# Optimization experiments

Measured on AMD Instinct MI355X. Metric: run time of the kernel, lower is better.

The kernel has to match this reference:

```python
import jax, jax.numpy as jnp
import numpy as np

D_MODEL = 1024
N_HEADS = 16
D_HEAD = D_MODEL // N_HEADS
D_FF = 4 * D_MODEL
B, T = 2, 2048
LN_EPS = 1e-5


def layer_norm(x, g, b):
    mu = jnp.mean(x, axis=-1, keepdims=True)
    var = jnp.mean(jnp.square(x - mu), axis=-1, keepdims=True)
    return (x - mu) * jax.lax.rsqrt(var + LN_EPS) * g + b


def setup_inputs() -> dict:
    key = jax.random.key(0)
    ks = jax.random.split(key, 8)
    s = lambda fan: 1.0 / np.sqrt(fan)
    return {
        "x": jax.random.normal(ks[0], (B, T, D_MODEL), dtype=jnp.float32),
        "ln1_g": jnp.ones((D_MODEL,), jnp.float32),
        "ln1_b": jnp.zeros((D_MODEL,), jnp.float32),
        "Wqkv": jax.random.normal(ks[1], (D_MODEL, 3 * D_MODEL), jnp.float32) * s(D_MODEL),
        "Wout": jax.random.normal(ks[2], (D_MODEL, D_MODEL), jnp.float32) * s(D_MODEL),
        "ln2_g": jnp.ones((D_MODEL,), jnp.float32),
        "ln2_b": jnp.zeros((D_MODEL,), jnp.float32),
        "W1": jax.random.normal(ks[3], (D_MODEL, D_FF), jnp.float32) * s(D_MODEL),
        "b1": jnp.zeros((D_FF,), jnp.float32),
        "W2": jax.random.normal(ks[4], (D_FF, D_MODEL), jnp.float32) * s(D_FF),
        "b2": jnp.zeros((D_MODEL,), jnp.float32),
    }


def attention(x, Wqkv, Wout):
    Bx, Tx, C = x.shape
    qkv = x @ Wqkv  # [B,T,3C]
    q, k, v = jnp.split(qkv, 3, axis=-1)
    q = q.reshape(Bx, Tx, N_HEADS, D_HEAD)
    k = k.reshape(Bx, Tx, N_HEADS, D_HEAD)
    v = v.reshape(Bx, Tx, N_HEADS, D_HEAD)
    scores = jnp.einsum('bqhd,bkhd->bhqk', q, k) / np.sqrt(D_HEAD).astype(np.float32)
    causal = jnp.tril(jnp.ones((Tx, Tx), dtype=bool))
    scores = jnp.where(causal, scores, -jnp.inf)
    attn = jax.nn.softmax(scores, axis=-1)
    out = jnp.einsum('bhqk,bkhd->bqhd', attn, v).reshape(Bx, Tx, C)
    return out @ Wout


def reference(x, ln1_g, ln1_b, Wqkv, Wout, ln2_g, ln2_b, W1, b1, W2, b2):
    x = x + attention(layer_norm(x, ln1_g, ln1_b), Wqkv, Wout)
    h = layer_norm(x, ln2_g, ln2_b)
    h = jax.nn.gelu(h @ W1 + b1, approximate=False) @ W2 + b2
    return x + h
```

## Files before the change

kernel.cpp:

```cpp
#include <hip/hip_runtime.h>
#include <math.h>

typedef __bf16 bf16;
typedef __bf16 bf16x4 __attribute__((ext_vector_type(4)));
typedef __bf16 bf16x8 __attribute__((ext_vector_type(8)));
typedef float  f32x4  __attribute__((ext_vector_type(4)));

#define MFMA16(a,b,c) __builtin_amdgcn_mfma_f32_16x16x32_bf16((a),(b),(c),0,0,0)

static __device__ __forceinline__ bf16x8 combine8(const bf16* plo, const bf16* phi) {
  bf16x4 lo = *(const bf16x4*)plo;
  bf16x4 hi = *(const bf16x4*)phi;
  return __builtin_shufflevector(lo, hi, 0, 1, 2, 3, 4, 5, 6, 7);
}

__global__ __launch_bounds__(256) void transpose_all(
    const float* __restrict__ Wqkv, bf16* __restrict__ WqkvT,
    const float* __restrict__ Wout, bf16* __restrict__ WoutT,
    const float* __restrict__ W1,   bf16* __restrict__ W1T,
    const float* __restrict__ W2,   bf16* __restrict__ W2T) {
  __shared__ float t[32][33];
  int b = blockIdx.x;
  const float* W; bf16* WT; int K, N, bx, by;
  if (b < 3072)      { W = Wqkv; WT = WqkvT; K = 1024; N = 3072;            bx = b % 96;  by = b / 96; }
  else if (b < 4096) { W = Wout; WT = WoutT; K = 1024; N = 1024; b -= 3072; bx = b % 32;  by = b / 32; }
  else if (b < 8192) { W = W1;   WT = W1T;   K = 1024; N = 4096; b -= 4096; bx = b % 128; by = b / 128; }
  else               { W = W2;   WT = W2T;   K = 4096; N = 1024; b -= 8192; bx = b % 32;  by = b / 32; }
  int n0 = bx * 32, k0 = by * 32;
  int tx = threadIdx.x, ty = threadIdx.y;
#pragma unroll
  for (int i = 0; i < 32; i += 8)
    t[ty + i][tx] = W[(size_t)(k0 + ty + i) * N + n0 + tx];
  __syncthreads();
#pragma unroll
  for (int i = 0; i < 32; i += 8)
    WT[(size_t)(n0 + ty + i) * K + k0 + tx] = (bf16)t[tx][ty + i];
}

__global__ __launch_bounds__(256) void ln_kernel(const float* __restrict__ X,
                                                 const float* __restrict__ g,
                                                 const float* __restrict__ bta,
                                                 bf16* __restrict__ out) {
  int row  = blockIdx.x * 4 + (threadIdx.x >> 6);
  int lane = threadIdx.x & 63;
  const float4* x4 = (const float4*)(X + (size_t)row * 1024);
  float4 v[4];
  float s = 0.f, ss = 0.f;
#pragma unroll
  for (int i = 0; i < 4; ++i) {
    v[i] = x4[i * 64 + lane];
    s  += v[i].x + v[i].y + v[i].z + v[i].w;
    ss += v[i].x * v[i].x + v[i].y * v[i].y + v[i].z * v[i].z + v[i].w * v[i].w;
  }
#pragma unroll
  for (int off = 1; off < 64; off <<= 1) {
    s  += __shfl_xor(s, off, 64);
    ss += __shfl_xor(ss, off, 64);
  }
  float mu  = s * (1.0f / 1024.0f);
  float var = ss * (1.0f / 1024.0f) - mu * mu;
  float rs  = rsqrtf(var + 1e-5f);
  bf16* orow = out + (size_t)row * 1024;
#pragma unroll
  for (int i = 0; i < 4; ++i) {
    int c = i * 256 + lane * 4;
    bf16x4 pk;
    pk[0] = (bf16)((v[i].x - mu) * rs * g[c + 0] + bta[c + 0]);
    pk[1] = (bf16)((v[i].y - mu) * rs * g[c + 1] + bta[c + 1]);
    pk[2] = (bf16)((v[i].z - mu) * rs * g[c + 2] + bta[c + 2]);
    pk[3] = (bf16)((v[i].w - mu) * rs * g[c + 3] + bta[c + 3]);
    *(bf16x4*)(orow + c) = pk;
  }
}

template <int NR>
static __device__ __forceinline__ void stage2(const bf16* const* srcs, int koff,
                                              unsigned char* lds_base, int wv) {
#pragma unroll
  for (int i = 0; i < NR; ++i)
    __builtin_amdgcn_global_load_lds(
        (const __attribute__((address_space(1))) void*)(srcs[i] + koff),
        (__attribute__((address_space(3))) void*)(lds_base + (wv * (NR * 8) + i * 8) * 128),
        16, 0, 0);
}

static __device__ __forceinline__ bf16x8 frag_ld(const unsigned char* lds_base,
                                                 int r, int u) {
  return *(const bf16x8*)(lds_base + r * 128 + (((u ^ (r & 7)) & 7) << 4));
}

static __device__ __forceinline__ float gelu_tanh(float v) {
  float t = 0.7978845608028654f * (v + 0.044715f * v * v * v);
  t = fminf(t, 15.0f);
  float e = __builtin_amdgcn_exp2f(2.8853900817779268f * t);
  float th = (e - 1.0f) * __builtin_amdgcn_rcpf(e + 1.0f);
  return 0.5f * v * (1.0f + th);
}

template <int EPI, int BM>
__global__ __launch_bounds__(256) void gemm_bt(const bf16* __restrict__ A,
                                               const bf16* __restrict__ BT,
                                               int K, int N, int gx,
                                               const float* __restrict__ bias,
                                               const float* __restrict__ res,
                                               bf16* __restrict__ outb,
                                               float* __restrict__ outf) {
  constexpr int MI = BM / 32;
  constexpr int ANR = BM / 32;
  __shared__ unsigned char smem[(BM + 128) * 128];
  int nwg = gridDim.x, bid = blockIdx.x;
  int nb = (bid & 7) * (nwg >> 3) + (bid >> 3);
  int bx = nb % gx, by = nb / gx;
  int brow = by * BM, bcol = bx * 128;
  int tid = threadIdx.x, wv = tid >> 6, lane = tid & 63;
  int l15 = lane & 15, l4 = lane >> 4;
  int wm = wv >> 1, wn = wv & 1;
  f32x4 acc[MI][4] = {};

  int sr = lane >> 3;
  int su = (lane & 7) ^ sr;
  const bf16* aptr[ANR];
#pragma unroll
  for (int i = 0; i < ANR; ++i)
    aptr[i] = A + (size_t)(brow + wv * (ANR * 8) + i * 8 + sr) * K + su * 8;
  const bf16* bptr[4];
#pragma unroll
  for (int i = 0; i < 4; ++i)
    bptr[i] = BT + (size_t)(bcol + wv * 32 + i * 8 + sr) * K + su * 8;

  unsigned char* As = smem;
  unsigned char* Bs = smem + BM * 128;
  for (int k0 = 0; k0 < K; k0 += 64) {
    stage2<ANR>(aptr, k0, As, wv);
    stage2<4>(bptr, k0, Bs, wv);
    __syncthreads();
#pragma unroll
    for (int ks = 0; ks < 2; ++ks) {
      bf16x8 af[MI], bfr[4];
#pragma unroll
      for (int mi = 0; mi < MI; ++mi)
        af[mi] = frag_ld(As, wm * (BM / 2) + mi * 16 + l15, ks * 4 + l4);
#pragma unroll
      for (int ni = 0; ni < 4; ++ni)
        bfr[ni] = frag_ld(Bs, wn * 64 + ni * 16 + l15, ks * 4 + l4);
#pragma unroll
      for (int mi = 0; mi < MI; ++mi)
#pragma unroll
        for (int ni = 0; ni < 4; ++ni)
          acc[mi][ni] = MFMA16(af[mi], bfr[ni], acc[mi][ni]);
    }
    __syncthreads();
  }
#pragma unroll
  for (int mi = 0; mi < MI; ++mi) {
#pragma unroll
    for (int ni = 0; ni < 4; ++ni) {
      int col  = bcol + wn * 64 + ni * 16 + l15;
      int row0 = brow + wm * (BM / 2) + mi * 16 + l4 * 4;
#pragma unroll
      for (int r = 0; r < 4; ++r) {
        int row = row0 + r;
        float v = acc[mi][ni][r];
        if (EPI == 1) {
          v += bias[col];
          v = gelu_tanh(v);
        }
        if (EPI == 2) v += res[(size_t)row * N + col];
        if (EPI == 3) v += bias[col] + res[(size_t)row * N + col];
        if (EPI == 0 || EPI == 1) outb[(size_t)row * N + col] = (bf16)v;
        else                      outf[(size_t)row * N + col] = v;
      }
    }
  }
}

__global__ __launch_bounds__(256) void pack_kv(const bf16* __restrict__ qkv,
                                               bf16* __restrict__ kpack,
                                               bf16* __restrict__ vpack) {
  int blk = blockIdx.x;
  int wv = threadIdx.x >> 6, lane = threadIdx.x & 63;
  int l15 = lane & 15, l4 = lane >> 4;
  int ch = (blk & 15) * 4 + wv;
  int bh = blk >> 4;
  int b = bh >> 4, h = bh & 15;
  const bf16* kq = qkv + (size_t)b * 2048 * 3072 + 1024 + h * 64;
  const bf16* vq = kq + 1024;
#pragma unroll
  for (int fr = 0; fr < 4; ++fr) {
    int key = ch * 32 + ((fr >> 1) << 4) + l15;
    int dbase = ((fr & 1) << 5) + l4 * 4;
    bf16x8 v = combine8(kq + (size_t)key * 3072 + dbase,
                        kq + (size_t)key * 3072 + dbase + 16);
    *(bf16x8*)(kpack + ((size_t)(bh * 64 + ch) * 4 + fr) * 512 + lane * 8) = v;
  }
#pragma unroll
  for (int db = 0; db < 4; ++db) {
    int d = db * 16 + l15;
    bf16x8 v;
#pragma unroll
    for (int j = 0; j < 8; ++j) {
      int key = ch * 32 + l4 * 4 + (j & 3) + ((j >> 2) << 4);
      v[j] = vq[(size_t)key * 3072 + d];
    }
    *(bf16x8*)(vpack + ((size_t)(bh * 64 + ch) * 4 + db) * 512 + lane * 8) = v;
  }
}

static __device__ __forceinline__ void proc_chunk(
    const bf16x8* __restrict__ kf, const bf16x8* __restrict__ vf,
    const bf16x8 (* __restrict__ qf)[2], f32x4 (* __restrict__ o)[4],
    float* __restrict__ lsum, bool diag, int l15, int l4) {
  const float SC = 0.125f * 1.4426950408889634f;
#pragma unroll
  for (int f = 0; f < 2; ++f) {
    f32x4 c0 = {0.f, 0.f, 0.f, 0.f}, c1 = {0.f, 0.f, 0.f, 0.f};
    c0 = MFMA16(kf[0], qf[f][0], c0);
    c0 = MFMA16(kf[1], qf[f][1], c0);
    c1 = MFMA16(kf[2], qf[f][0], c1);
    c1 = MFMA16(kf[3], qf[f][1], c1);
    bf16x8 pf;
    float ls = 0.f;
#pragma unroll
    for (int r = 0; r < 4; ++r) {
      float e0 = __builtin_amdgcn_exp2f(c0[r] * SC);
      float e1 = __builtin_amdgcn_exp2f(c1[r] * SC);
      if (diag) {
        int qg = f * 16 + l15;
        int key = l4 * 4 + r;
        if (key > qg)      e0 = 0.f;
        if (key + 16 > qg) e1 = 0.f;
      }
      ls += e0 + e1;
      pf[r]     = (bf16)e0;
      pf[4 + r] = (bf16)e1;
    }
    lsum[f] += ls;
    o[f][0] = MFMA16(vf[0], pf, o[f][0]);
    o[f][1] = MFMA16(vf[1], pf, o[f][1]);
    o[f][2] = MFMA16(vf[2], pf, o[f][2]);
    o[f][3] = MFMA16(vf[3], pf, o[f][3]);
  }
}

__global__ __launch_bounds__(256) void attn_kernel(const bf16* __restrict__ qkv,
                                                   const bf16* __restrict__ kpack,
                                                   const bf16* __restrict__ vpack,
                                                   bf16* __restrict__ attn_out) {
  __shared__ f32x4 obuf[48 * 64];
  __shared__ float lbuf[12 * 64];
  int bid = blockIdx.x;
  int nb = (bid & 7) * 128 + (bid >> 3);
  int bh = nb >> 5, j = nb & 31;
  int b = bh >> 4, h = bh & 15;
  int wv = threadIdx.x >> 6, lane = threadIdx.x & 63;
  int l15 = lane & 15, l4 = lane >> 4;
  int qc[2] = {j, 63 - j};
  const bf16* base = qkv + (size_t)b * 2048 * 3072;
  int d0 = l4 * 4;
  bf16x8 qf[2][2][2];
#pragma unroll
  for (int c = 0; c < 2; ++c)
#pragma unroll
    for (int f = 0; f < 2; ++f) {
      const bf16* qp = base + (size_t)(qc[c] * 32 + f * 16 + l15) * 3072 + h * 64;
      qf[c][f][0] = combine8(qp + d0,      qp + d0 + 16);
      qf[c][f][1] = combine8(qp + d0 + 32, qp + d0 + 48);
    }
  const bf16* kp0 = kpack + (size_t)bh * 64 * 2048 + lane * 8;
  const bf16* vp0 = vpack + (size_t)bh * 64 * 2048 + lane * 8;

  f32x4 o[2][2][4] = {};
  float lsum[2][2] = {};

  for (int ch = wv; ch <= qc[1]; ch += 4) {
    const bf16* kp = kp0 + (size_t)ch * 2048;
    const bf16* vp = vp0 + (size_t)ch * 2048;
    bf16x8 kf[4], vf[4];
    kf[0] = *(const bf16x8*)(kp);
    kf[1] = *(const bf16x8*)(kp + 512);
    kf[2] = *(const bf16x8*)(kp + 1024);
    kf[3] = *(const bf16x8*)(kp + 1536);
    vf[0] = *(const bf16x8*)(vp);
    vf[1] = *(const bf16x8*)(vp + 512);
    vf[2] = *(const bf16x8*)(vp + 1024);
    vf[3] = *(const bf16x8*)(vp + 1536);
    if (ch <= qc[0])
      proc_chunk(kf, vf, qf[0], o[0], lsum[0], ch == qc[0], l15, l4);
    proc_chunk(kf, vf, qf[1], o[1], lsum[1], ch == qc[1], l15, l4);
  }

#pragma unroll
  for (int s = 0; s < 4; ++s) {
    if (s == wv) continue;
    int sp = s - (s > wv ? 1 : 0);
    int c = s >> 1, f = s & 1;
#pragma unroll
    for (int db = 0; db < 4; ++db)
      obuf[((wv * 3 + sp) * 4 + db) * 64 + lane] = o[c][f][db];
    lbuf[(wv * 3 + sp) * 64 + lane] = lsum[c][f];
  }
  __syncthreads();
  {
    int c = wv >> 1, f = wv & 1;
    f32x4 osum[4];
#pragma unroll
    for (int db = 0; db < 4; ++db) osum[db] = o[c][f][db];
    float l = lsum[c][f];
#pragma unroll
    for (int ww = 0; ww < 4; ++ww) {
      if (ww == wv) continue;
      int sp = wv - (wv > ww ? 1 : 0);
#pragma unroll
      for (int db = 0; db < 4; ++db)
        osum[db] += obuf[((ww * 3 + sp) * 4 + db) * 64 + lane];
      l += lbuf[(ww * 3 + sp) * 64 + lane];
    }
    l += __shfl_xor(l, 16, 64);
    l += __shfl_xor(l, 32, 64);
    float inv = 1.0f / l;
    bf16* orow = attn_out +
                 (size_t)(b * 2048 + qc[c] * 32 + f * 16 + l15) * 1024 +
                 h * 64 + l4 * 4;
#pragma unroll
    for (int db = 0; db < 4; ++db) {
      bf16x4 pk;
      pk[0] = (bf16)(osum[db][0] * inv);
      pk[1] = (bf16)(osum[db][1] * inv);
      pk[2] = (bf16)(osum[db][2] * inv);
      pk[3] = (bf16)(osum[db][3] * inv);
      *(bf16x4*)(orow + db * 16) = pk;
    }
  }
}

extern "C" void kernel_launch(void* const* d_in, const int* in_sizes, int n_in,
                              void* d_out, int out_size, void* d_ws, size_t ws_size,
                              hipStream_t stream) {
  const float* x     = (const float*)d_in[0];
  const float* ln1g  = (const float*)d_in[1];
  const float* ln1b  = (const float*)d_in[2];
  const float* Wqkv  = (const float*)d_in[3];
  const float* Wout  = (const float*)d_in[4];
  const float* ln2g  = (const float*)d_in[5];
  const float* ln2b  = (const float*)d_in[6];
  const float* W1    = (const float*)d_in[7];
  const float* b1    = (const float*)d_in[8];
  const float* W2    = (const float*)d_in[9];
  const float* b2    = (const float*)d_in[10];
  float* out = (float*)d_out;

  char* p = (char*)d_ws;
  bf16* WqkvT = (bf16*)p; p += (size_t)3072 * 1024 * 2;
  bf16* WoutT = (bf16*)p; p += (size_t)1024 * 1024 * 2;
  bf16* W1T   = (bf16*)p; p += (size_t)4096 * 1024 * 2;
  bf16* W2T   = (bf16*)p; p += (size_t)1024 * 4096 * 2;
  bf16* hbuf  = (bf16*)p; p += (size_t)4096 * 1024 * 2;
  bf16* aobuf = (bf16*)p; p += (size_t)4096 * 1024 * 2;
  bf16* big   = (bf16*)p; p += (size_t)4096 * 4096 * 2;

  bf16* kpack = big + (size_t)4096 * 3072;
  bf16* vpack = hbuf;

  transpose_all<<<12288, dim3(32, 8), 0, stream>>>(Wqkv, WqkvT, Wout, WoutT,
                                                   W1, W1T, W2, W2T);

  ln_kernel<<<1024, 256, 0, stream>>>(x, ln1g, ln1b, hbuf);
  gemm_bt<0, 128><<<768, 256, 0, stream>>>(hbuf, WqkvT, 1024, 3072, 24,
                                           nullptr, nullptr, big, nullptr);
  pack_kv<<<512, 256, 0, stream>>>(big, kpack, vpack);
  attn_kernel<<<1024, 256, 0, stream>>>(big, kpack, vpack, aobuf);
  gemm_bt<2, 64><<<512, 256, 0, stream>>>(aobuf, WoutT, 1024, 1024, 8,
                                          nullptr, x, nullptr, out);
  ln_kernel<<<1024, 256, 0, stream>>>(out, ln2g, ln2b, hbuf);
  gemm_bt<1, 128><<<1024, 256, 0, stream>>>(hbuf, W1T, 1024, 4096, 32,
                                            b1, nullptr, big, nullptr);
  gemm_bt<3, 64><<<512, 256, 0, stream>>>(big, W2T, 4096, 1024, 8,
                                          b2, out, nullptr, out);
}
```

Before: 235.0 us.

## Double-buffer GEMM shared tiles and shrink attention reduction LDS

The GEMM now keeps two shared-memory tile buffers and stages the next K-slice into the alternate buffer while computing the current one, with one barrier per iteration instead of two. This lets global-to-LDS loads overlap MFMA work. The attention epilogue reduces the two query chunks in two passes, so the cross-wave buffers shrink from 48 to 8 slots; this should help occupancy at the cost of an extra barrier. The doubled GEMM LDS footprint may lower occupancy.

After: 214.3 us. -8.8%, faster.

```diff
diff --git a/kernel.cpp b/kernel.cpp
--- a/kernel.cpp
+++ b/kernel.cpp
@@ -107,7 +107,8 @@
                                                float* __restrict__ outf) {
   constexpr int MI = BM / 32;
   constexpr int ANR = BM / 32;
-  __shared__ unsigned char smem[(BM + 128) * 128];
+  constexpr int TILE = (BM + 128) * 128;
+  __shared__ unsigned char smem[TILE * 2];
   int nwg = gridDim.x, bid = blockIdx.x;
   int nb = (bid & 7) * (nwg >> 3) + (bid >> 3);
   int bx = nb % gx, by = nb / gx;
@@ -128,12 +129,19 @@
   for (int i = 0; i < 4; ++i)
     bptr[i] = BT + (size_t)(bcol + wv * 32 + i * 8 + sr) * K + su * 8;
 
-  unsigned char* As = smem;
-  unsigned char* Bs = smem + BM * 128;
+  stage2<ANR>(aptr, 0, smem, wv);
+  stage2<4>(bptr, 0, smem + BM * 128, wv);
+  __syncthreads();
+  int cur = 0;
   for (int k0 = 0; k0 < K; k0 += 64) {
-    stage2<ANR>(aptr, k0, As, wv);
-    stage2<4>(bptr, k0, Bs, wv);
-    __syncthreads();
+    unsigned char* sc = smem + cur * TILE;
+    if (k0 + 64 < K) {
+      unsigned char* sn = smem + (cur ^ 1) * TILE;
+      stage2<ANR>(aptr, k0 + 64, sn, wv);
+      stage2<4>(bptr, k0 + 64, sn + BM * 128, wv);
+    }
+    unsigned char* As = sc;
+    unsigned char* Bs = sc + BM * 128;
 #pragma unroll
     for (int ks = 0; ks < 2; ++ks) {
       bf16x8 af[MI], bfr[4];
@@ -150,6 +158,7 @@
           acc[mi][ni] = MFMA16(af[mi], bfr[ni], acc[mi][ni]);
     }
     __syncthreads();
+    cur ^= 1;
   }
 #pragma unroll
   for (int mi = 0; mi < MI; ++mi) {
@@ -246,8 +255,8 @@
                                                    const bf16* __restrict__ kpack,
                                                    const bf16* __restrict__ vpack,
                                                    bf16* __restrict__ attn_out) {
-  __shared__ f32x4 obuf[48 * 64];
-  __shared__ float lbuf[12 * 64];
+  __shared__ f32x4 obuf[8 * 4 * 64];
+  __shared__ float lbuf[8 * 64];
   int bid = blockIdx.x;
   int nb = (bid & 7) * 128 + (bid >> 3);
   int bh = nb >> 5, j = nb & 31;
@@ -290,45 +299,49 @@
   }
 
 #pragma unroll
-  for (int s = 0; s < 4; ++s) {
-    if (s == wv) continue;
-    int sp = s - (s > wv ? 1 : 0);
-    int c = s >> 1, f = s & 1;
-#pragma unroll
-    for (int db = 0; db < 4; ++db)
-      obuf[((wv * 3 + sp) * 4 + db) * 64 + lane] = o[c][f][db];
-    lbuf[(wv * 3 + sp) * 64 + lane] = lsum[c][f];
-  }
-  __syncthreads();
-  {
-    int c = wv >> 1, f = wv & 1;
-    f32x4 osum[4];
-#pragma unroll
-    for (int db = 0; db < 4; ++db) osum[db] = o[c][f][db];
-    float l = lsum[c][f];
-#pragma unroll
-    for (int ww = 0; ww < 4; ++ww) {
-      if (ww == wv) continue;
-      int sp = wv - (wv > ww ? 1 : 0);
-#pragma unroll
-      for (int db = 0; db < 4; ++db)
-        osum[db] += obuf[((ww * 3 + sp) * 4 + db) * 64 + lane];
-      l += lbuf[(ww * 3 + sp) * 64 + lane];
-    }
-    l += __shfl_xor(l, 16, 64);
-    l += __shfl_xor(l, 32, 64);
-    float inv = 1.0f / l;
-    bf16* orow = attn_out +
-                 (size_t)(b * 2048 + qc[c] * 32 + f * 16 + l15) * 1024 +
-                 h * 64 + l4 * 4;
-#pragma unroll
-    for (int db = 0; db < 4; ++db) {
-      bf16x4 pk;
-      pk[0] = (bf16)(osum[db][0] * inv);
-      pk[1] = (bf16)(osum[db][1] * inv);
-      pk[2] = (bf16)(osum[db][2] * inv);
-      pk[3] = (bf16)(osum[db][3] * inv);
-      *(bf16x4*)(orow + db * 16) = pk;
+  for (int c = 0; c < 2; ++c) {
+    if (c) __syncthreads();
+#pragma unroll
+    for (int f = 0; f < 2; ++f) {
+      if (wv != c * 2 + f) {
+        int slot = wv * 2 + f;
+#pragma unroll
+        for (int db = 0; db < 4; ++db)
+          obuf[(slot * 4 + db) * 64 + lane] = o[c][f][db];
+        lbuf[slot * 64 + lane] = lsum[c][f];
+      }
+    }
+    __syncthreads();
+    if ((wv >> 1) == c) {
+      int f = wv & 1;
+      f32x4 osum[4];
+#pragma unroll
+      for (int db = 0; db < 4; ++db) osum[db] = o[c][f][db];
+      float l = lsum[c][f];
+#pragma unroll
+      for (int ww = 0; ww < 4; ++ww) {
+        if (ww == wv) continue;
+        int slot = ww * 2 + f;
+#pragma unroll
+        for (int db = 0; db < 4; ++db)
+          osum[db] += obuf[(slot * 4 + db) * 64 + lane];
+        l += lbuf[slot * 64 + lane];
+      }
+      l += __shfl_xor(l, 16, 64);
+      l += __shfl_xor(l, 32, 64);
+      float inv = 1.0f / l;
+      bf16* orow = attn_out +
+                   (size_t)(b * 2048 + qc[c] * 32 + f * 16 + l15) * 1024 +
+                   h * 64 + l4 * 4;
+#pragma unroll
+      for (int db = 0; db < 4; ++db) {
+        bf16x4 pk;
+        pk[0] = (bf16)(osum[db][0] * inv);
+        pk[1] = (bf16)(osum[db][1] * inv);
+        pk[2] = (bf16)(osum[db][2] * inv);
+        pk[3] = (bf16)(osum[db][3] * inv);
+        *(bf16x4*)(orow + db * 16) = pk;
+      }
     }
   }
 }
```
